# Kernel optimization log

Measured on AMD Instinct MI355X. Metric: run time of the kernel, lower is better.

The kernel has to match this reference:

```python
import jax, jax.numpy as jnp
import numpy as np

B, E, H, S, V, K = 128, 512, 512, 2048, 83, 3
PAD = 82


def _pos_emb(n, e):
    pos = jnp.arange(n, dtype=jnp.float32)[:, None]                      # [n,1]
    k = jnp.exp(-jnp.log(10000.0) * jnp.arange(0, e, 2, dtype=jnp.float32) / e)  # [e/2]
    arg = pos * k                                                        # [n,e/2]
    pe = jnp.stack([jnp.sin(arg), jnp.cos(arg)], axis=-1).reshape(n, e)  # interleave sin/cos
    return pe.T                                                          # [e,n]


def setup_inputs() -> dict:
    key = jax.random.key(0)
    ks = jax.random.split(key, 8)
    return {
        "encoder_output": jax.random.normal(ks[0], (B, H, S), dtype=jnp.float32),
        "encoder_total": jax.random.normal(ks[1], (B, H, S), dtype=jnp.float32),
        "decoder_input": jax.random.randint(ks[2], (B,), 0, V),
        "count": 0,
        "emb": jax.random.normal(ks[3], (V, E), dtype=jnp.float32) * 0.02,
        "conv_w": jax.random.normal(ks[4], (2 * H, E, K), dtype=jnp.float32) * 0.02,
        "conv_b": jnp.zeros((2 * H,), dtype=jnp.float32),
        "lin2_w": jax.random.normal(ks[5], (V, H), dtype=jnp.float32) * 0.02,
        "lin2_b": jnp.zeros((V,), dtype=jnp.float32),
    }


def reference(encoder_output, encoder_total, decoder_input, count, emb, conv_w, conv_b, lin2_w, lin2_b):
    # count==0 first-step path; dropout is identity (inference).
    pe3 = _pos_emb(K, E)                                    # [E,K]

    def layer(dec_in):
        # dec_in: [B,E,K]
        xp = dec_in + pe3[None]                             # positional embedding add
        y = jnp.einsum('bek,oek->bo', xp, conv_w) + conv_b  # valid conv1d, out length 1 -> [B,2H]
        a, b = jnp.split(y, 2, axis=1)
        glu = a * jax.nn.sigmoid(b)                         # [B,H]
        d = glu + xp[:, :, -1]                              # residual with last (pe-added) column
        scores = jnp.einsum('bh,bhs->bs', d, encoder_output)
        attn = jax.nn.softmax(scores, axis=-1)              # [B,S]
        c = jnp.einsum('bs,bhs->bh', attn, encoder_total)   # [B,H]
        h = glu + c
        logits = h @ lin2_w.T + lin2_b                      # [B,V]
        return h, jax.nn.log_softmax(logits, axis=-1)

    x = emb[decoder_input][:, :, None]                      # [B,E,1]
    pad_col = jnp.broadcast_to(emb[PAD][None, :, None], (B, E, 1))
    dec1 = jnp.concatenate([pad_col, pad_col, x], axis=2)   # [B,E,3]

    h1, _ = layer(dec1)                                     # n_l = 0
    dec2 = jnp.concatenate([dec1[:, :, :2], h1[:, :, None]], axis=2)
    h2, _ = layer(dec2)                                     # n_l = 1
    dec3 = jnp.concatenate([dec1[:, :, :2], h2[:, :, None]], axis=2)
    h3, ls3 = layer(dec3)                                   # n_l = 2

    return (jax.nn.softmax(h3, axis=1)[:, :, None],         # [B,H,1]
            ls3[:, None, :])                                # [B,1,V]
```

## Files before the change

### kernel.cpp

```cpp
#include <hip/hip_runtime.h>
#include <math.h>

#define B_   128
#define E_   512
#define H_   512
#define S_   2048
#define V_   83
#define PAD_ 82

__device__ __forceinline__ float pe_val(int e, int n) {
    float freq = expf(-9.210340371976184f * (float)(e & ~1) * (1.0f / 512.0f));
    float a = (float)n * freq;
    return (e & 1) ? cosf(a) : sinf(a);
}


__global__ void k_prep(const float* __restrict__ cw, float* __restrict__ W2t) {
    int idx = blockIdx.x * 256 + threadIdx.x;
    int e = idx >> 10, o = idx & 1023;
    W2t[idx] = cw[o * 1536 + e * 3 + 2];
}

__global__ void k_base(const float* __restrict__ cw, const float* __restrict__ emb,
                       float* __restrict__ base) {
    int t = threadIdx.x;
    __shared__ float x0[512], x1[512];
    for (int j = t; j < 512; j += 256) {
        float ep = emb[PAD_ * 512 + j];
        x0[j] = ep + pe_val(j, 0);
        x1[j] = ep + pe_val(j, 1);
    }
    __syncthreads();
    int o = blockIdx.x * 256 + t;
    float acc = 0.f;
    for (int e = 0; e < 512; ++e) {
        acc += x0[e] * cw[o * 1536 + e * 3 + 0];
        acc += x1[e] * cw[o * 1536 + e * 3 + 1];
    }
    base[o] = acc;
}


__global__ void k_x(int first, const int* __restrict__ tok, const float* __restrict__ emb,
                    const float* __restrict__ h, float* __restrict__ xcol) {
    int idx = blockIdx.x * 256 + threadIdx.x;
    int b = idx >> 9, e = idx & 511;
    float v = first ? emb[tok[b] * 512 + e] : h[idx];
    xcol[idx] = v + pe_val(e, 2);
}

__global__ void k_y(const float* __restrict__ xcol, const float* __restrict__ W2t,
                    const float* __restrict__ base, const float* __restrict__ cb,
                    float* __restrict__ y) {
    int oc = blockIdx.x, bq = blockIdx.y, t = threadIdx.x;
    __shared__ float xs[4][512];
    for (int j = t; j < 2048; j += 256) xs[j >> 9][j & 511] = xcol[bq * 2048 + j];
    __syncthreads();
    int o = oc * 256 + t;
    float init = base[o] + cb[o];
    float a0 = init, a1 = init, a2 = init, a3 = init;
    for (int e = 0; e < 512; ++e) {
        float w = W2t[e * 1024 + o];
        a0 += xs[0][e] * w; a1 += xs[1][e] * w;
        a2 += xs[2][e] * w; a3 += xs[3][e] * w;
    }
    int b0 = bq * 4;
    y[(size_t)(b0 + 0) * 1024 + o] = a0;
    y[(size_t)(b0 + 1) * 1024 + o] = a1;
    y[(size_t)(b0 + 2) * 1024 + o] = a2;
    y[(size_t)(b0 + 3) * 1024 + o] = a3;
}

__global__ void k_glud(const float* __restrict__ y, const float* __restrict__ xcol,
                       float* __restrict__ glu, float* __restrict__ dv) {
    int idx = blockIdx.x * 256 + threadIdx.x;
    int b = idx >> 9, hh = idx & 511;
    float ya = y[(size_t)b * 1024 + hh];
    float yb = y[(size_t)b * 1024 + 512 + hh];
    float g = ya / (1.0f + expf(-yb));
    glu[idx] = g;
    dv[idx] = g + xcol[idx];
}

__global__ void k_scores(const float* __restrict__ dv, const float* __restrict__ enc,
                         float* __restrict__ attn) {
    int sc = blockIdx.x, b = blockIdx.y, t = threadIdx.x;
    int wave = t >> 6, lane = t & 63;
    __shared__ float dl[512];
    __shared__ float red[1024];
    for (int j = t; j < 512; j += 256) dl[j] = dv[b * 512 + j];
    __syncthreads();
    const float* ep = enc + (size_t)b * 512 * 2048 + sc * 256 + lane * 4;
    float a0 = 0, a1 = 0, a2 = 0, a3 = 0;
    int h0 = wave * 128;
    for (int hh = 0; hh < 128; ++hh) {
        float4 v = *(const float4*)(ep + (size_t)(h0 + hh) * 2048);
        float dh = dl[h0 + hh];
        a0 += dh * v.x; a1 += dh * v.y;
        a2 += dh * v.z; a3 += dh * v.w;
    }
    int sl = wave * 256 + lane * 4;
    red[sl + 0] = a0; red[sl + 1] = a1; red[sl + 2] = a2; red[sl + 3] = a3;
    __syncthreads();
    float s = red[t] + red[256 + t] + red[512 + t] + red[768 + t];
    attn[b * 2048 + sc * 256 + t] = s;
}

__global__ void k_softmax(float* __restrict__ attn) {
    int b = blockIdx.x, t = threadIdx.x;
    float v[8];
    float m = -1e30f;
    for (int i = 0; i < 8; ++i) { v[i] = attn[b * 2048 + i * 256 + t]; m = fmaxf(m, v[i]); }
    __shared__ float r[256];
    r[t] = m; __syncthreads();
    for (int s = 128; s > 0; s >>= 1) { if (t < s) r[t] = fmaxf(r[t], r[t + s]); __syncthreads(); }
    float M = r[0]; __syncthreads();
    float sum = 0.f;
    for (int i = 0; i < 8; ++i) { v[i] = expf(v[i] - M); sum += v[i]; }
    r[t] = sum; __syncthreads();
    for (int s = 128; s > 0; s >>= 1) { if (t < s) r[t] += r[t + s]; __syncthreads(); }
    float inv = 1.0f / r[0];
    for (int i = 0; i < 8; ++i) attn[b * 2048 + i * 256 + t] = v[i] * inv;
}

__global__ void k_c(const float* __restrict__ attn, const float* __restrict__ enc,
                    const float* __restrict__ glu, float* __restrict__ hbuf) {
    int t = threadIdx.x;
    int widx = blockIdx.x * 4 + (t >> 6);
    int lane = t & 63;
    int b = widx >> 9, hh = widx & 511;
    const float* vp = enc + (size_t)(b * 512 + hh) * 2048;
    const float* ap = attn + b * 2048;
    float acc = 0.f;
    #pragma unroll
    for (int it = 0; it < 8; ++it) {
        int s = it * 256 + lane * 4;
        float4 w = *(const float4*)(vp + s);
        float4 p = *(const float4*)(ap + s);
        acc += p.x * w.x + p.y * w.y + p.z * w.z + p.w * w.w;
    }
    #pragma unroll
    for (int off = 32; off > 0; off >>= 1) acc += __shfl_down(acc, off, 64);
    if (lane == 0) hbuf[b * 512 + hh] = glu[b * 512 + hh] + acc;
}


__global__ void k_logits(const float* __restrict__ h, const float* __restrict__ l2w,
                         const float* __restrict__ l2b, float* __restrict__ out) {
    int b = blockIdx.x, t = threadIdx.x;
    __shared__ float hl[512];
    for (int j = t; j < 512; j += 128) hl[j] = h[b * 512 + j];
    __syncthreads();
    float acc = 0.f;
    if (t < V_) {
        acc = l2b[t];
        for (int e = 0; e < 512; ++e) acc += hl[e] * l2w[t * 512 + e];
    }
    __shared__ float r[128];
    r[t] = (t < V_) ? acc : -1e30f; __syncthreads();
    for (int s = 64; s > 0; s >>= 1) { if (t < s) r[t] = fmaxf(r[t], r[t + s]); __syncthreads(); }
    float M = r[0]; __syncthreads();
    r[t] = (t < V_) ? expf(acc - M) : 0.f; __syncthreads();
    for (int s = 64; s > 0; s >>= 1) { if (t < s) r[t] += r[t + s]; __syncthreads(); }
    float L = M + logf(r[0]);
    if (t < V_) out[65536 + b * V_ + t] = acc - L;
}

__global__ void k_out0(const float* __restrict__ h, float* __restrict__ out) {
    int b = blockIdx.x, t = threadIdx.x;
    float v0 = h[b * 512 + t], v1 = h[b * 512 + 256 + t];
    __shared__ float r[256];
    r[t] = fmaxf(v0, v1); __syncthreads();
    for (int s = 128; s > 0; s >>= 1) { if (t < s) r[t] = fmaxf(r[t], r[t + s]); __syncthreads(); }
    float M = r[0]; __syncthreads();
    float e0 = expf(v0 - M), e1 = expf(v1 - M);
    r[t] = e0 + e1; __syncthreads();
    for (int s = 128; s > 0; s >>= 1) { if (t < s) r[t] += r[t + s]; __syncthreads(); }
    float inv = 1.0f / r[0];
    out[b * 512 + t] = e0 * inv;
    out[b * 512 + 256 + t] = e1 * inv;
}


extern "C" void kernel_launch(void* const* d_in, const int* in_sizes, int n_in,
                              void* d_out, int out_size, void* d_ws, size_t ws_size,
                              hipStream_t stream) {
    const float* enc_out = (const float*)d_in[0];
    const float* enc_tot = (const float*)d_in[1];
    const int*   tok     = (const int*)d_in[2];
    const float* emb     = (const float*)d_in[4];
    const float* conv_w  = (const float*)d_in[5];
    const float* conv_b  = (const float*)d_in[6];
    const float* l2w     = (const float*)d_in[7];
    const float* l2b     = (const float*)d_in[8];
    float* out = (float*)d_out;
    float* ws = (float*)d_ws;

    float* W2t  = ws;
    float* base = W2t + 524288;
    float* xcol = base + 1024;
    float* yb   = xcol + 65536;
    float* glu  = yb + 131072;
    float* dv   = glu + 65536;
    float* attn = dv + 65536;
    float* hbuf = attn + 262144;

    k_prep<<<2048, 256, 0, stream>>>(conv_w, W2t);
    k_base<<<4, 256, 0, stream>>>(conv_w, emb, base);

    for (int L = 0; L < 3; ++L) {
        k_x<<<256, 256, 0, stream>>>(L == 0 ? 1 : 0, tok, emb, hbuf, xcol);
        k_y<<<dim3(4, 32), 256, 0, stream>>>(xcol, W2t, base, conv_b, yb);
        k_glud<<<256, 256, 0, stream>>>(yb, xcol, glu, dv);
        k_scores<<<dim3(8, 128), 256, 0, stream>>>(dv, enc_out, attn);
        k_softmax<<<128, 256, 0, stream>>>(attn);
        k_c<<<16384, 256, 0, stream>>>(attn, enc_tot, glu, hbuf);
    }

    k_logits<<<128, 128, 0, stream>>>(hbuf, l2w, l2b, out);
    k_out0<<<128, 256, 0, stream>>>(hbuf, out);
}
```

Before: 722.4 us.

## Fuse GLU into scores/context kernels, split scores over H chunks, coalesce base GEMV

```diff
diff --git a/kernel.cpp b/kernel.cpp
--- a/kernel.cpp
+++ b/kernel.cpp
@@ -21,32 +21,48 @@
     W2t[idx] = cw[o * 1536 + e * 3 + 2];
 }
 
-__global__ void k_base(const float* __restrict__ cw, const float* __restrict__ emb,
-                       float* __restrict__ base) {
-    int t = threadIdx.x;
-    __shared__ float x0[512], x1[512];
-    for (int j = t; j < 512; j += 256) {
-        float ep = emb[PAD_ * 512 + j];
-        x0[j] = ep + pe_val(j, 0);
-        x1[j] = ep + pe_val(j, 1);
-    }
-    __syncthreads();
-    int o = blockIdx.x * 256 + t;
+__global__ void k_misc(const float* __restrict__ emb, float* __restrict__ pe2,
+                       float* __restrict__ x01i) {
+    int e = threadIdx.x;
+    float freq = expf(-9.210340371976184f * (float)(e & ~1) * (1.0f / 512.0f));
+    float p0 = (e & 1) ? 1.0f : 0.0f;
+    float p1 = (e & 1) ? cosf(freq) : sinf(freq);
+    float p2 = (e & 1) ? cosf(2.0f * freq) : sinf(2.0f * freq);
+    pe2[e] = p2;
+    float ep = emb[PAD_ * 512 + e];
+    x01i[e * 3 + 0] = ep + p0;
+    x01i[e * 3 + 1] = ep + p1;
+    x01i[e * 3 + 2] = 0.0f;
+}
+
+__global__ void k_base3(const float* __restrict__ cw, const float* __restrict__ x01i,
+                        float* __restrict__ base) {
+    int t = threadIdx.x, w = t >> 6, lane = t & 63;
+    __shared__ float xs[1536];
+    for (int j = t; j < 1536; j += 256) xs[j] = x01i[j];
+    __syncthreads();
+    int o = blockIdx.x * 4 + w;
+    const float* rp = cw + (size_t)o * 1536 + lane * 4;
     float acc = 0.f;
-    for (int e = 0; e < 512; ++e) {
-        acc += x0[e] * cw[o * 1536 + e * 3 + 0];
-        acc += x1[e] * cw[o * 1536 + e * 3 + 1];
-    }
-    base[o] = acc;
+    #pragma unroll
+    for (int j = 0; j < 6; ++j) {
+        float4 v = *(const float4*)(rp + j * 256);
+        const float* xp = &xs[lane * 4 + j * 256];
+        acc += v.x * xp[0] + v.y * xp[1] + v.z * xp[2] + v.w * xp[3];
+    }
+    #pragma unroll
+    for (int off = 32; off > 0; off >>= 1) acc += __shfl_down(acc, off, 64);
+    if (lane == 0) base[o] = acc;
 }
 
 
 __global__ void k_x(int first, const int* __restrict__ tok, const float* __restrict__ emb,
-                    const float* __restrict__ h, float* __restrict__ xcol) {
+                    const float* __restrict__ h, const float* __restrict__ pe2,
+                    float* __restrict__ xcol) {
     int idx = blockIdx.x * 256 + threadIdx.x;
     int b = idx >> 9, e = idx & 511;
     float v = first ? emb[tok[b] * 512 + e] : h[idx];
-    xcol[idx] = v + pe_val(e, 2);
+    xcol[idx] = v + pe2[e];
 }
 
 __global__ void k_y(const float* __restrict__ xcol, const float* __restrict__ W2t,
@@ -71,46 +87,64 @@
     y[(size_t)(b0 + 3) * 1024 + o] = a3;
 }
 
-__global__ void k_glud(const float* __restrict__ y, const float* __restrict__ xcol,
-                       float* __restrict__ glu, float* __restrict__ dv) {
-    int idx = blockIdx.x * 256 + threadIdx.x;
-    int b = idx >> 9, hh = idx & 511;
-    float ya = y[(size_t)b * 1024 + hh];
-    float yb = y[(size_t)b * 1024 + 512 + hh];
-    float g = ya / (1.0f + expf(-yb));
-    glu[idx] = g;
-    dv[idx] = g + xcol[idx];
-}
-
-__global__ void k_scores(const float* __restrict__ dv, const float* __restrict__ enc,
-                         float* __restrict__ attn) {
-    int sc = blockIdx.x, b = blockIdx.y, t = threadIdx.x;
-    int wave = t >> 6, lane = t & 63;
-    __shared__ float dl[512];
-    __shared__ float red[1024];
-    for (int j = t; j < 512; j += 256) dl[j] = dv[b * 512 + j];
-    __syncthreads();
-    const float* ep = enc + (size_t)b * 512 * 2048 + sc * 256 + lane * 4;
-    float a0 = 0, a1 = 0, a2 = 0, a3 = 0;
-    int h0 = wave * 128;
-    for (int hh = 0; hh < 128; ++hh) {
-        float4 v = *(const float4*)(ep + (size_t)(h0 + hh) * 2048);
-        float dh = dl[h0 + hh];
-        a0 += dh * v.x; a1 += dh * v.y;
-        a2 += dh * v.z; a3 += dh * v.w;
-    }
-    int sl = wave * 256 + lane * 4;
-    red[sl + 0] = a0; red[sl + 1] = a1; red[sl + 2] = a2; red[sl + 3] = a3;
-    __syncthreads();
-    float s = red[t] + red[256 + t] + red[512 + t] + red[768 + t];
-    attn[b * 2048 + sc * 256 + t] = s;
-}
-
-__global__ void k_softmax(float* __restrict__ attn) {
+__global__ void k_scores2(const float* __restrict__ y, const float* __restrict__ xcol,
+                          const float* __restrict__ enc, float* __restrict__ part) {
+    int hc = blockIdx.x, b = blockIdx.y, t = threadIdx.x;
+    int w = t >> 6, lane = t & 63;
+    __shared__ float dl[64];
+    __shared__ float red[4 * 2048];
+    if (t < 64) {
+        int hg = hc * 64 + t;
+        float ya = y[b * 1024 + hg];
+        float yb_ = y[b * 1024 + 512 + hg];
+        float g = ya / (1.0f + expf(-yb_));
+        dl[t] = g + xcol[b * 512 + hg];
+    }
+    __syncthreads();
+    float4 a[8];
+    #pragma unroll
+    for (int j = 0; j < 8; ++j) a[j] = make_float4(0.f, 0.f, 0.f, 0.f);
+    const float* bp = enc + ((size_t)b * 512 + hc * 64 + w * 16) * 2048 + lane * 4;
+    for (int r = 0; r < 16; ++r) {
+        float dh = dl[w * 16 + r];
+        const float* rp = bp + (size_t)r * 2048;
+        #pragma unroll
+        for (int j = 0; j < 8; ++j) {
+            float4 v = *(const float4*)(rp + j * 256);
+            a[j].x += dh * v.x; a[j].y += dh * v.y;
+            a[j].z += dh * v.z; a[j].w += dh * v.w;
+        }
+    }
+    #pragma unroll
+    for (int j = 0; j < 8; ++j)
+        *(float4*)&red[w * 2048 + j * 256 + lane * 4] = a[j];
+    __syncthreads();
+    #pragma unroll
+    for (int k = 0; k < 2; ++k) {
+        int s = t * 4 + k * 1024;
+        float4 s0 = *(const float4*)&red[0 * 2048 + s];
+        float4 s1 = *(const float4*)&red[1 * 2048 + s];
+        float4 s2 = *(const float4*)&red[2 * 2048 + s];
+        float4 s3 = *(const float4*)&red[3 * 2048 + s];
+        float4 o4 = make_float4(s0.x + s1.x + s2.x + s3.x,
+                                s0.y + s1.y + s2.y + s3.y,
+                                s0.z + s1.z + s2.z + s3.z,
+                                s0.w + s1.w + s2.w + s3.w);
+        *(float4*)&part[(size_t)hc * 262144 + b * 2048 + s] = o4;
+    }
+}
+
+__global__ void k_softmax2(const float* __restrict__ part, float* __restrict__ attn) {
     int b = blockIdx.x, t = threadIdx.x;
     float v[8];
     float m = -1e30f;
-    for (int i = 0; i < 8; ++i) { v[i] = attn[b * 2048 + i * 256 + t]; m = fmaxf(m, v[i]); }
+    for (int i = 0; i < 8; ++i) {
+        int s = i * 256 + t;
+        float acc = 0.f;
+        #pragma unroll
+        for (int hc = 0; hc < 8; ++hc) acc += part[(size_t)hc * 262144 + b * 2048 + s];
+        v[i] = acc; m = fmaxf(m, acc);
+    }
     __shared__ float r[256];
     r[t] = m; __syncthreads();
     for (int s = 128; s > 0; s >>= 1) { if (t < s) r[t] = fmaxf(r[t], r[t + s]); __syncthreads(); }
@@ -123,8 +157,8 @@
     for (int i = 0; i < 8; ++i) attn[b * 2048 + i * 256 + t] = v[i] * inv;
 }
 
-__global__ void k_c(const float* __restrict__ attn, const float* __restrict__ enc,
-                    const float* __restrict__ glu, float* __restrict__ hbuf) {
+__global__ void k_c2(const float* __restrict__ attn, const float* __restrict__ enc,
+                     const float* __restrict__ y, float* __restrict__ hbuf) {
     int t = threadIdx.x;
     int widx = blockIdx.x * 4 + (t >> 6);
     int lane = t & 63;
@@ -141,7 +175,12 @@
     }
     #pragma unroll
     for (int off = 32; off > 0; off >>= 1) acc += __shfl_down(acc, off, 64);
-    if (lane == 0) hbuf[b * 512 + hh] = glu[b * 512 + hh] + acc;
+    if (lane == 0) {
+        float ya = y[b * 1024 + hh];
+        float yb_ = y[b * 1024 + 512 + hh];
+        float g = ya / (1.0f + expf(-yb_));
+        hbuf[b * 512 + hh] = g + acc;
+    }
 }
 
 
@@ -198,23 +237,24 @@
 
     float* W2t  = ws;
     float* base = W2t + 524288;
-    float* xcol = base + 1024;
+    float* pe2  = base + 1024;
+    float* x01i = pe2 + 512;
+    float* xcol = x01i + 1536;
     float* yb   = xcol + 65536;
-    float* glu  = yb + 131072;
-    float* dv   = glu + 65536;
-    float* attn = dv + 65536;
-    float* hbuf = attn + 262144;
+    float* attn = yb + 131072;
+    float* part = attn + 262144;
+    float* hbuf = part + 2097152;
 
     k_prep<<<2048, 256, 0, stream>>>(conv_w, W2t);
-    k_base<<<4, 256, 0, stream>>>(conv_w, emb, base);
+    k_misc<<<1, 512, 0, stream>>>(emb, pe2, x01i);
+    k_base3<<<256, 256, 0, stream>>>(conv_w, x01i, base);
 
     for (int L = 0; L < 3; ++L) {
-        k_x<<<256, 256, 0, stream>>>(L == 0 ? 1 : 0, tok, emb, hbuf, xcol);
+        k_x<<<256, 256, 0, stream>>>(L == 0 ? 1 : 0, tok, emb, hbuf, pe2, xcol);
         k_y<<<dim3(4, 32), 256, 0, stream>>>(xcol, W2t, base, conv_b, yb);
-        k_glud<<<256, 256, 0, stream>>>(yb, xcol, glu, dv);
-        k_scores<<<dim3(8, 128), 256, 0, stream>>>(dv, enc_out, attn);
-        k_softmax<<<128, 256, 0, stream>>>(attn);
-        k_c<<<16384, 256, 0, stream>>>(attn, enc_tot, glu, hbuf);
+        k_scores2<<<dim3(8, 128), 256, 0, stream>>>(yb, xcol, enc_out, part);
+        k_softmax2<<<128, 256, 0, stream>>>(part, attn);
+        k_c2<<<16384, 256, 0, stream>>>(attn, enc_tot, yb, hbuf);
     }
 
     k_logits<<<128, 128, 0, stream>>>(hbuf, l2w, l2b, out);
```

New measurement: 706.2 us. 2.2% less time.
